# Performance work log

Measured on AMD Instinct MI355X. Metric: run time of the kernel, lower is better.

The kernel has to match this reference:

```python
import jax, jax.numpy as jnp
import numpy as np

D, E, H, K = 1024, 8, 1024, 2          # d_model, num_experts, hidden_size, top_k
NUM_LAYERS, LB_W, Z_W = 16, 0.01, 0.001
B, S = 2, 2048


def setup_inputs() -> dict:
    key = jax.random.key(0)
    ks = jax.random.split(key, 8)
    s = lambda d: 1.0 / np.sqrt(d)
    return {
        "x": jax.random.normal(ks[0], (B, S, D), jnp.float32),
        "w_router": jax.random.normal(ks[1], (D, E), jnp.float32) * s(D),
        "w1": jax.random.normal(ks[2], (E, D, H), jnp.float32) * s(D),
        "w3": jax.random.normal(ks[3], (E, D, H), jnp.float32) * s(D),
        "w2": jax.random.normal(ks[4], (E, H, D), jnp.float32) * s(H),
        "sw1": jax.random.normal(ks[5], (D, H), jnp.float32) * s(D),
        "sw3": jax.random.normal(ks[6], (D, H), jnp.float32) * s(D),
        "sw2": jax.random.normal(ks[7], (H, D), jnp.float32) * s(H),
    }


def reference(x, w_router, w1, w3, w2, sw1, sw3, sw2):
    b, s_len, _ = x.shape
    xt = x.reshape(-1, D)                       # (N, D) flattened tokens
    n_tok = xt.shape[0]

    # ---- router: softmax over experts, then top-k ----
    logits = xt @ w_router                      # (N, E)
    probs = jax.nn.softmax(logits, axis=-1)
    weights, indices = jax.lax.top_k(probs, K)  # (N, K)

    # combine weights scattered back to dense (N, E) form
    onehot = jax.nn.one_hot(indices, E, dtype=x.dtype)    # (N, K, E)
    cw = jnp.einsum("nk,nke->ne", weights, onehot)       # (N, E)
    counts = jnp.sum(onehot, axis=(0, 1))                 # (E,) tokens per expert

    # ---- expert SwiGLU MLPs (dense dispatch, weighted combine) ----
    g = jnp.einsum("nd,edh->neh", xt, w1)                 # (N, E, H)
    u = jnp.einsum("nd,edh->neh", xt, w3)
    h = jax.nn.silu(g) * u
    eout = jnp.einsum("neh,ehd->ned", h, w2)              # (N, E, D)
    out = jnp.einsum("ne,ned->nd", cw, eout)              # (N, D)

    # ---- shared expert, weighted-sum combine with top_k ----
    shared = (jax.nn.silu(xt @ sw1) * (xt @ sw3)) @ sw2   # (N, D)
    out = (out * K + shared) / (K + 1)

    # ---- aux losses (training mode) ----
    logits32 = logits.astype(jnp.float32)
    scale = E * LB_W / (NUM_LAYERS * n_tok * K)
    lb_loss = scale * jnp.dot(counts.astype(jnp.float32),
                              jax.nn.softmax(logits32, axis=-1).sum(axis=0))
    z_loss = jnp.mean(jnp.square(jax.nn.logsumexp(logits32, axis=-1))) * Z_W

    return out.reshape(b, s_len, D), lb_loss, z_loss
```

## Files before the change

### kernel.cpp

```cpp
#include <hip/hip_runtime.h>

#define NTOK 4096
#define NEXP 8
#define MAXTILES 104

typedef __attribute__((ext_vector_type(8))) short short8;
typedef __attribute__((ext_vector_type(4))) float f32x4;
typedef __attribute__((ext_vector_type(4))) unsigned int uint4v;
typedef __attribute__((ext_vector_type(2))) unsigned int uint2v;

__device__ __forceinline__ unsigned short f2bf(float f) {
  union { float f; unsigned u; } v; v.f = f;
  unsigned u = v.u;
  return (unsigned short)((u + 0x7FFFu + ((u >> 16) & 1u)) >> 16);
}

__device__ __forceinline__ void gll16(const void* g, void* l) {
  __builtin_amdgcn_global_load_lds((const __attribute__((address_space(1))) void*)g,
                                   (__attribute__((address_space(3))) void*)l, 16, 0, 0);
}

__global__ __launch_bounds__(256) void cvt_t_all_k(
    const float* __restrict__ w1, const float* __restrict__ w3, const float* __restrict__ w2,
    const float* __restrict__ sw1, const float* __restrict__ sw3, const float* __restrict__ sw2,
    unsigned short* __restrict__ dst ) {
  __shared__ unsigned short tile[64][65];
  int z = blockIdx.z;
  const float* S;
  if (z < 8) S = w1 + (size_t)z * 1048576;
  else if (z < 16) S = w3 + (size_t)(z - 8) * 1048576;
  else if (z < 24) S = w2 + (size_t)(z - 16) * 1048576;
  else S = (z == 24) ? sw1 : (z == 25) ? sw3 : sw2;
  unsigned short* Dp = dst + (size_t)z * 1048576;
  int r0 = blockIdx.y * 64, c0 = blockIdx.x * 64;
  int t = threadIdx.x;
  int r = t >> 2, cb = (t & 3) * 16;
  const float* sp = S + (size_t)(r0 + r) * 1024 + c0 + cb;
  f32x4 v0 = ((const f32x4*)sp)[0], v1 = ((const f32x4*)sp)[1];
  f32x4 v2 = ((const f32x4*)sp)[2], v3 = ((const f32x4*)sp)[3];
#pragma unroll
  for (int j = 0; j < 4; ++j) {
    tile[r][cb + j] = f2bf(v0[j]);
    tile[r][cb + 4 + j] = f2bf(v1[j]);
    tile[r][cb + 8 + j] = f2bf(v2[j]);
    tile[r][cb + 12 + j] = f2bf(v3[j]);
  }
  __syncthreads();
  unsigned short* dp = Dp + (size_t)(c0 + r) * 1024 + r0 + cb;
  uint4v o0, o1;
#pragma unroll
  for (int j = 0; j < 4; ++j) {
    o0[j] = (unsigned)tile[cb + 2 * j][r] | ((unsigned)tile[cb + 2 * j + 1][r] << 16);
    o1[j] = (unsigned)tile[cb + 8 + 2 * j][r] | ((unsigned)tile[cb + 9 + 2 * j][r] << 16);
  }
  ((uint4v*)dp)[0] = o0;
  ((uint4v*)dp)[1] = o1;
}

__global__ __launch_bounds__(256) void router_k(
    const float* __restrict__ x, const float* __restrict__ wr, unsigned short* __restrict__ xb,
    int* __restrict__ rec, float* __restrict__ wts, float* __restrict__ probs,
    float* __restrict__ lsebuf) {
  int t = threadIdx.x, lane = t & 63, wv = t >> 6;
  int tok = blockIdx.x * 4 + wv;
  const f32x4* x4 = (const f32x4*)(x + (size_t)tok * 1024);
  f32x4 xv[4];
#pragma unroll
  for (int j = 0; j < 4; ++j) xv[j] = x4[j * 64 + lane];

  unsigned short* xo = xb + (size_t)tok * 1024;
#pragma unroll
  for (int j = 0; j < 4; ++j) {
    uint2v o;
    o[0] = (unsigned)f2bf(xv[j][0]) | ((unsigned)f2bf(xv[j][1]) << 16);
    o[1] = (unsigned)f2bf(xv[j][2]) | ((unsigned)f2bf(xv[j][3]) << 16);
    *(uint2v*)(xo + j * 256 + lane * 4) = o;
  }

  float acc[NEXP];
#pragma unroll
  for (int e = 0; e < NEXP; ++e) acc[e] = 0.f;
#pragma unroll
  for (int j = 0; j < 4; ++j) {
    int base = j * 256 + lane * 4;
#pragma unroll
    for (int c = 0; c < 4; ++c) {
      float xf = xv[j][c];
      const f32x4* wp = (const f32x4*)(wr + (size_t)(base + c) * NEXP);
      f32x4 w0 = wp[0], w1 = wp[1];
#pragma unroll
      for (int e = 0; e < 4; ++e) { acc[e] += xf * w0[e]; acc[4 + e] += xf * w1[e]; }
    }
  }
#pragma unroll
  for (int off = 32; off > 0; off >>= 1) {
#pragma unroll
    for (int e = 0; e < NEXP; ++e) acc[e] += __shfl_xor(acc[e], off);
  }

  float mx = acc[0];
#pragma unroll
  for (int e = 1; e < NEXP; ++e) mx = fmaxf(mx, acc[e]);
  float s = 0.f;
#pragma unroll
  for (int e = 0; e < NEXP; ++e) s += __expf(acc[e] - mx);
  float inv = 1.f / s;

  if (lane < NEXP) probs[(size_t)tok * NEXP + lane] = __expf(acc[lane] - mx) * inv;
  if (lane == 0) {
    int i0 = 0; float v0 = acc[0];
#pragma unroll
    for (int e = 1; e < NEXP; ++e) if (acc[e] > v0) { v0 = acc[e]; i0 = e; }
    int i1 = -1; float v1 = -3.4e38f;
#pragma unroll
    for (int e = 0; e < NEXP; ++e) if (e != i0 && acc[e] > v1) { v1 = acc[e]; i1 = e; }
    rec[tok] = i0 | (i1 << 8);
    wts[2 * tok] = __expf(v0 - mx) * inv;
    wts[2 * tok + 1] = __expf(v1 - mx) * inv;
    lsebuf[tok] = mx + __logf(s);
  }
}

__global__ __launch_bounds__(256) void build_k(
    const int* __restrict__ rec, const float* __restrict__ wts, const float* __restrict__ probs,
    const float* __restrict__ lsebuf,
    int* __restrict__ tlist, float* __restrict__ wlist,
    int* __restrict__ counts, float* __restrict__ probsum, float* __restrict__ zsum) {
  __shared__ int lcnt[NEXP];
  __shared__ int gbase[NEXP];
  __shared__ float wProb[4][NEXP];
  __shared__ float wZ[4];
  int t = threadIdx.x, lane = t & 63, wv = t >> 6;
  if (t < NEXP) lcnt[t] = 0;
  __syncthreads();

  int tok = blockIdx.x * 256 + t;
  int r = rec[tok];
  int i0 = r & 255, i1 = (r >> 8) & 255;
  float w0 = wts[2 * tok], w1 = wts[2 * tok + 1];
  int p0 = atomicAdd(&lcnt[i0], 1);
  int p1 = atomicAdd(&lcnt[i1], 1);

  f32x4 pr0 = ((const f32x4*)(probs + (size_t)tok * NEXP))[0];
  f32x4 pr1 = ((const f32x4*)(probs + (size_t)tok * NEXP))[1];
  float lv = lsebuf[tok];
  float z = lv * lv;
#pragma unroll
  for (int off = 32; off > 0; off >>= 1) {
#pragma unroll
    for (int c = 0; c < 4; ++c) {
      pr0[c] += __shfl_xor(pr0[c], off);
      pr1[c] += __shfl_xor(pr1[c], off);
    }
    z += __shfl_xor(z, off);
  }
  if (lane == 0) {
#pragma unroll
    for (int c = 0; c < 4; ++c) { wProb[wv][c] = pr0[c]; wProb[wv][4 + c] = pr1[c]; }
    wZ[wv] = z;
  }
  __syncthreads();

  if (t < NEXP) {
    gbase[t] = atomicAdd(&counts[t], lcnt[t]);
    atomicAdd(&probsum[t], wProb[0][t] + wProb[1][t] + wProb[2][t] + wProb[3][t]);
  }
  if (t == 0) atomicAdd(zsum, wZ[0] + wZ[1] + wZ[2] + wZ[3]);
  __syncthreads();

  int q0 = gbase[i0] + p0, q1 = gbase[i1] + p1;
  tlist[i0 * NTOK + q0] = tok;
  wlist[i0 * NTOK + q0] = w0;
  tlist[i1 * NTOK + q1] = tok;
  wlist[i1 * NTOK + q1] = w1;
}

__global__ void scan_k(const int* __restrict__ counts, int* __restrict__ ebase, int* __restrict__ tiles) {
  if (threadIdx.x == 0 && blockIdx.x == 0) {
    int a = 0, t = 0;
    for (int e = 0; e < NEXP; ++e) {
      ebase[e] = a;
      int nt = (counts[e] + 127) >> 7;
      for (int i = 0; i < nt; ++i) tiles[t++] = (e << 16) | i;
      a += nt * 128;
    }
    ebase[NEXP] = a;
    for (int i = 0; i < 32; ++i) tiles[t++] = (NEXP << 16) | i;
    ebase[NEXP + 1] = a + NTOK;
    while (t < MAXTILES) tiles[t++] = -1;
  }
}

__global__ __launch_bounds__(256, 3) void gemm1_k(
    const unsigned short* __restrict__ xb,
    const unsigned short* __restrict__ w1T, const unsigned short* __restrict__ w3T,
    const unsigned short* __restrict__ sw1T, const unsigned short* __restrict__ sw3T,
    unsigned short* __restrict__ hout,
    const int* __restrict__ tlist, const int* __restrict__ counts,
    const int* __restrict__ ebase, const int* __restrict__ tiles) {
  int td = tiles[blockIdx.y];
  if (td < 0) return;
  const int e = td >> 16;
  const int m0 = (td & 0xFFFF) << 7;
  const int n0 = blockIdx.x * 64;
  const bool sh = (e == NEXP);
  const int n_e = sh ? NTOK : counts[e];
  const int hb = ebase[e];
  const unsigned short* B1p = sh ? sw1T : w1T + (size_t)e * 1048576;
  const unsigned short* B3p = sh ? sw3T : w3T + (size_t)e * 1048576;
  const int* listp = tlist + e * NTOK;

  __shared__ unsigned short As[128 * 64], Bs1[64 * 64], Bs3[64 * 64];
  const int tid = threadIdx.x, lane = tid & 63, wv = tid >> 6;
  const int wrw = wv >> 1, wc = wv & 1, l16 = lane & 15, lq = lane >> 4;

  const unsigned short* ga[4];
#pragma unroll
  for (int i = 0; i < 4; ++i) {
    int c = tid + i * 256;
    int r = c >> 3, ks = (c & 7) ^ (r & 7);
    int ar = m0 + r;
    int rowA = sh ? ar : (ar < n_e ? (listp[ar] & 0xFFFF) : 0);
    ga[i] = xb + (size_t)rowA * 1024 + ks * 8;
  }
  const unsigned short* gb[2];
  const unsigned short* gc[2];
#pragma unroll
  for (int i = 0; i < 2; ++i) {
    int c = tid + i * 256;
    int r = c >> 3, ks = (c & 7) ^ (r & 7);
    gb[i] = B1p + (size_t)(n0 + r) * 1024 + ks * 8;
    gc[i] = B3p + (size_t)(n0 + r) * 1024 + ks * 8;
  }
  unsigned short* lA[4];
#pragma unroll
  for (int i = 0; i < 4; ++i) lA[i] = As + i * 2048 + wv * 512;
  unsigned short* lB[2] = {Bs1 + wv * 512, Bs1 + 2048 + wv * 512};
  unsigned short* lC[2] = {Bs3 + wv * 512, Bs3 + 2048 + wv * 512};

  f32x4 accg[4][2], accu[4][2];
#pragma unroll
  for (int mi = 0; mi < 4; ++mi)
#pragma unroll
    for (int ni = 0; ni < 2; ++ni)
#pragma unroll
      for (int r = 0; r < 4; ++r) { accg[mi][ni][r] = 0.f; accu[mi][ni][r] = 0.f; }

  for (int k0 = 0; k0 < 1024; k0 += 64) {
#pragma unroll
    for (int i = 0; i < 4; ++i) { gll16(ga[i], lA[i]); ga[i] += 64; }
#pragma unroll
    for (int i = 0; i < 2; ++i) { gll16(gb[i], lB[i]); gb[i] += 64; gll16(gc[i], lC[i]); gc[i] += 64; }
    __syncthreads();
#pragma unroll
    for (int kh = 0; kh < 2; ++kh) {
      short8 af[4], b1f[2], b3f[2];
#pragma unroll
      for (int mi = 0; mi < 4; ++mi) {
        int R = wrw * 64 + mi * 16 + l16;
        int s = (kh * 4 + lq) ^ (R & 7);
        af[mi] = *(const short8*)&As[R * 64 + s * 8];
      }
#pragma unroll
      for (int ni = 0; ni < 2; ++ni) {
        int R = wc * 32 + ni * 16 + l16;
        int s = (kh * 4 + lq) ^ (R & 7);
        b1f[ni] = *(const short8*)&Bs1[R * 64 + s * 8];
        b3f[ni] = *(const short8*)&Bs3[R * 64 + s * 8];
      }
#pragma unroll
      for (int mi = 0; mi < 4; ++mi)
#pragma unroll
        for (int ni = 0; ni < 2; ++ni) {
          accg[mi][ni] = __builtin_amdgcn_mfma_f32_16x16x32_bf16(af[mi], b1f[ni], accg[mi][ni], 0, 0, 0);
          accu[mi][ni] = __builtin_amdgcn_mfma_f32_16x16x32_bf16(af[mi], b3f[ni], accu[mi][ni], 0, 0, 0);
        }
    }
    __syncthreads();
  }

#pragma unroll
  for (int mi = 0; mi < 4; ++mi)
#pragma unroll
    for (int ni = 0; ni < 2; ++ni) {
      int col = n0 + wc * 32 + ni * 16 + l16;
#pragma unroll
      for (int r = 0; r < 4; ++r) {
        int row = m0 + wrw * 64 + mi * 16 + lq * 4 + r;
        float g = accg[mi][ni][r], u = accu[mi][ni][r];
        float h = g / (1.f + __expf(-g)) * u;
        hout[(size_t)(hb + row) * 1024 + col] = (row < n_e) ? f2bf(h) : (unsigned short)0;
      }
    }
}

__global__ __launch_bounds__(256, 3) void gemm2_k(
    const unsigned short* __restrict__ hbuf,
    const unsigned short* __restrict__ w2T, const unsigned short* __restrict__ sw2T,
    float* __restrict__ out,
    const int* __restrict__ tlist, const float* __restrict__ wlist,
    const int* __restrict__ counts, const int* __restrict__ ebase, const int* __restrict__ tiles) {
  int td = tiles[blockIdx.y];
  if (td < 0) return;
  const int e = td >> 16;
  const int m0 = (td & 0xFFFF) << 7;
  const int n0 = blockIdx.x * 128;
  const bool sh = (e == NEXP);
  const int n_e = sh ? NTOK : counts[e];
  const int hb = ebase[e];
  const unsigned short* Bp = sh ? sw2T : w2T + (size_t)e * 1048576;
  const int* listp = tlist + e * NTOK;

  __shared__ unsigned short As[128 * 64], Bs[128 * 64];
  const int tid = threadIdx.x, lane = tid & 63, wv = tid >> 6;
  const int wrw = wv >> 1, wc = wv & 1, l16 = lane & 15, lq = lane >> 4;

  const unsigned short* ga[4];
  const unsigned short* gb[4];
#pragma unroll
  for (int i = 0; i < 4; ++i) {
    int c = tid + i * 256;
    int r = c >> 3, ks = (c & 7) ^ (r & 7);
    ga[i] = hbuf + (size_t)(hb + m0 + r) * 1024 + ks * 8;
    gb[i] = Bp + (size_t)(n0 + r) * 1024 + ks * 8;
  }
  unsigned short* lA[4];
  unsigned short* lB[4];
#pragma unroll
  for (int i = 0; i < 4; ++i) {
    lA[i] = As + i * 2048 + wv * 512;
    lB[i] = Bs + i * 2048 + wv * 512;
  }

  f32x4 acc[4][4];
#pragma unroll
  for (int mi = 0; mi < 4; ++mi)
#pragma unroll
    for (int ni = 0; ni < 4; ++ni)
#pragma unroll
      for (int r = 0; r < 4; ++r) acc[mi][ni][r] = 0.f;

  for (int k0 = 0; k0 < 1024; k0 += 64) {
#pragma unroll
    for (int i = 0; i < 4; ++i) {
      gll16(ga[i], lA[i]); ga[i] += 64;
      gll16(gb[i], lB[i]); gb[i] += 64;
    }
    __syncthreads();
#pragma unroll
    for (int kh = 0; kh < 2; ++kh) {
      short8 af[4], bf[4];
#pragma unroll
      for (int mi = 0; mi < 4; ++mi) {
        int R = wrw * 64 + mi * 16 + l16;
        int s = (kh * 4 + lq) ^ (R & 7);
        af[mi] = *(const short8*)&As[R * 64 + s * 8];
      }
#pragma unroll
      for (int ni = 0; ni < 4; ++ni) {
        int R = wc * 64 + ni * 16 + l16;
        int s = (kh * 4 + lq) ^ (R & 7);
        bf[ni] = *(const short8*)&Bs[R * 64 + s * 8];
      }
#pragma unroll
      for (int mi = 0; mi < 4; ++mi)
#pragma unroll
        for (int ni = 0; ni < 4; ++ni)
          acc[mi][ni] = __builtin_amdgcn_mfma_f32_16x16x32_bf16(af[mi], bf[ni], acc[mi][ni], 0, 0, 0);
    }
    __syncthreads();
  }

#pragma unroll
  for (int mi = 0; mi < 4; ++mi)
#pragma unroll
    for (int r = 0; r < 4; ++r) {
      int row = m0 + wrw * 64 + mi * 16 + lq * 4 + r;
      if (sh) {
        float* yp = out + (size_t)row * 1024 + n0 + wc * 64 + l16;
#pragma unroll
        for (int ni = 0; ni < 4; ++ni) atomicAdd(&yp[ni * 16], acc[mi][ni][r] * (1.f / 3.f));
      } else if (row < n_e) {
        int tok = listp[row] & 0xFFFF;
        float wt = wlist[e * NTOK + row] * (2.f / 3.f);
        float* yp = out + (size_t)tok * 1024 + n0 + wc * 64 + l16;
#pragma unroll
        for (int ni = 0; ni < 4; ++ni) atomicAdd(&yp[ni * 16], wt * acc[mi][ni][r]);
      }
    }
}

__global__ void losses_k(const int* __restrict__ counts, const float* __restrict__ probsum,
                         const float* __restrict__ zsum, float* __restrict__ out) {
  if (threadIdx.x == 0 && blockIdx.x == 0) {
    float dot = 0.f;
    for (int e = 0; e < NEXP; ++e) dot += (float)counts[e] * probsum[e];
    out[0] = 6.103515625e-7f * dot;
    out[1] = zsum[0] * (0.001f / 4096.f);
  }
}

extern "C" void kernel_launch(void* const* d_in, const int* in_sizes, int n_in,
                              void* d_out, int out_size, void* d_ws, size_t ws_size,
                              hipStream_t stream) {
  const float* x   = (const float*)d_in[0];
  const float* wrt = (const float*)d_in[1];
  const float* w1  = (const float*)d_in[2];
  const float* w3  = (const float*)d_in[3];
  const float* w2  = (const float*)d_in[4];
  const float* sw1 = (const float*)d_in[5];
  const float* sw3 = (const float*)d_in[6];
  const float* sw2 = (const float*)d_in[7];
  float* out = (float*)d_out;

  char* p = (char*)d_ws;
  auto alloc = [&](size_t b) { char* r = p; p += (b + 255) & ~(size_t)255; return r; };
  unsigned short* xb   = (unsigned short*)alloc((size_t)NTOK * 1024 * 2);
  unsigned short* w1T  = (unsigned short*)alloc((size_t)27 * 1048576 * 2);
  unsigned short* w3T  = w1T + (size_t)8 * 1048576;
  unsigned short* w2T  = w3T + (size_t)8 * 1048576;
  unsigned short* sw1T = w2T + (size_t)8 * 1048576;
  unsigned short* sw3T = sw1T + 1048576;
  unsigned short* sw2T = sw3T + 1048576;
  unsigned short* hbuf = (unsigned short*)alloc((size_t)13312 * 1024 * 2);
  int* tlist    = (int*)alloc((size_t)NEXP * NTOK * 4);
  float* wlist  = (float*)alloc((size_t)NEXP * NTOK * 4);
  int* rec      = (int*)alloc((size_t)NTOK * 4);
  float* wts    = (float*)alloc((size_t)NTOK * 2 * 4);
  float* probs  = (float*)alloc((size_t)NTOK * NEXP * 4);
  float* lsebuf = (float*)alloc((size_t)NTOK * 4);
  int* tiles    = (int*)alloc(MAXTILES * 4);
  int* ebase    = (int*)alloc(256);
  char* stats   = alloc(768);
  int* counts   = (int*)stats;
  float* probsum = (float*)(stats + 256);
  float* zsum    = (float*)(stats + 512);

  (void)hipMemsetAsync(stats, 0, 768, stream);
  (void)hipMemsetAsync(out, 0, (size_t)out_size * 4, stream);

  cvt_t_all_k<<<dim3(16, 16, 27), 256, 0, stream>>>(w1, w3, w2, sw1, sw3, sw2, w1T);
  router_k<<<1024, 256, 0, stream>>>(x, wrt, xb, rec, wts, probs, lsebuf);
  build_k<<<16, 256, 0, stream>>>(rec, wts, probs, lsebuf, tlist, wlist, counts, probsum, zsum);
  scan_k<<<1, 64, 0, stream>>>(counts, ebase, tiles);
  gemm1_k<<<dim3(16, MAXTILES), 256, 0, stream>>>(xb, w1T, w3T, sw1T, sw3T, hbuf, tlist, counts, ebase, tiles);
  gemm2_k<<<dim3(8, MAXTILES), 256, 0, stream>>>(hbuf, w2T, sw2T, out, tlist, wlist, counts, ebase, tiles);
  losses_k<<<1, 64, 0, stream>>>(counts, probsum, zsum, out + (size_t)NTOK * 1024);
}
```

Measured before the change: 326.7 us.

## Fuse prep kernels, single-block routing build, replace atomic combine with staged sum

Merges weight conversion and the router into one launch, and folds the build, scan and loss kernels into a single 1024-thread block. This drops the memsets and several small launches. gemm2 no longer does float atomicAdds into the output. It writes each of the top-k and shared contributions to a separate slice of a 3-slot fp32 buffer, and a new combine kernel sums them. The aim is to remove atomic contention and launch overhead, at the cost of writing and reading an extra 48MB buffer. The single-block build also serialises the routing scatter.

```diff
diff --git a/kernel.cpp b/kernel.cpp
--- a/kernel.cpp
+++ b/kernel.cpp
@@ -20,174 +20,174 @@
                                    (__attribute__((address_space(3))) void*)l, 16, 0, 0);
 }
 
-__global__ __launch_bounds__(256) void cvt_t_all_k(
+__global__ __launch_bounds__(256) void prep_k(
     const float* __restrict__ w1, const float* __restrict__ w3, const float* __restrict__ w2,
     const float* __restrict__ sw1, const float* __restrict__ sw3, const float* __restrict__ sw2,
-    unsigned short* __restrict__ dst ) {
-  __shared__ unsigned short tile[64][65];
-  int z = blockIdx.z;
-  const float* S;
-  if (z < 8) S = w1 + (size_t)z * 1048576;
-  else if (z < 16) S = w3 + (size_t)(z - 8) * 1048576;
-  else if (z < 24) S = w2 + (size_t)(z - 16) * 1048576;
-  else S = (z == 24) ? sw1 : (z == 25) ? sw3 : sw2;
-  unsigned short* Dp = dst + (size_t)z * 1048576;
-  int r0 = blockIdx.y * 64, c0 = blockIdx.x * 64;
-  int t = threadIdx.x;
-  int r = t >> 2, cb = (t & 3) * 16;
-  const float* sp = S + (size_t)(r0 + r) * 1024 + c0 + cb;
-  f32x4 v0 = ((const f32x4*)sp)[0], v1 = ((const f32x4*)sp)[1];
-  f32x4 v2 = ((const f32x4*)sp)[2], v3 = ((const f32x4*)sp)[3];
-#pragma unroll
-  for (int j = 0; j < 4; ++j) {
-    tile[r][cb + j] = f2bf(v0[j]);
-    tile[r][cb + 4 + j] = f2bf(v1[j]);
-    tile[r][cb + 8 + j] = f2bf(v2[j]);
-    tile[r][cb + 12 + j] = f2bf(v3[j]);
-  }
-  __syncthreads();
-  unsigned short* dp = Dp + (size_t)(c0 + r) * 1024 + r0 + cb;
-  uint4v o0, o1;
-#pragma unroll
-  for (int j = 0; j < 4; ++j) {
-    o0[j] = (unsigned)tile[cb + 2 * j][r] | ((unsigned)tile[cb + 2 * j + 1][r] << 16);
-    o1[j] = (unsigned)tile[cb + 8 + 2 * j][r] | ((unsigned)tile[cb + 9 + 2 * j][r] << 16);
-  }
-  ((uint4v*)dp)[0] = o0;
-  ((uint4v*)dp)[1] = o1;
-}
-
-__global__ __launch_bounds__(256) void router_k(
+    unsigned short* __restrict__ dst,
     const float* __restrict__ x, const float* __restrict__ wr, unsigned short* __restrict__ xb,
     int* __restrict__ rec, float* __restrict__ wts, float* __restrict__ probs,
     float* __restrict__ lsebuf) {
-  int t = threadIdx.x, lane = t & 63, wv = t >> 6;
-  int tok = blockIdx.x * 4 + wv;
-  const f32x4* x4 = (const f32x4*)(x + (size_t)tok * 1024);
-  f32x4 xv[4];
-#pragma unroll
-  for (int j = 0; j < 4; ++j) xv[j] = x4[j * 64 + lane];
-
-  unsigned short* xo = xb + (size_t)tok * 1024;
-#pragma unroll
-  for (int j = 0; j < 4; ++j) {
-    uint2v o;
-    o[0] = (unsigned)f2bf(xv[j][0]) | ((unsigned)f2bf(xv[j][1]) << 16);
-    o[1] = (unsigned)f2bf(xv[j][2]) | ((unsigned)f2bf(xv[j][3]) << 16);
-    *(uint2v*)(xo + j * 256 + lane * 4) = o;
-  }
-
-  float acc[NEXP];
-#pragma unroll
-  for (int e = 0; e < NEXP; ++e) acc[e] = 0.f;
-#pragma unroll
-  for (int j = 0; j < 4; ++j) {
-    int base = j * 256 + lane * 4;
-#pragma unroll
-    for (int c = 0; c < 4; ++c) {
-      float xf = xv[j][c];
-      const f32x4* wp = (const f32x4*)(wr + (size_t)(base + c) * NEXP);
-      f32x4 w0 = wp[0], w1 = wp[1];
-#pragma unroll
-      for (int e = 0; e < 4; ++e) { acc[e] += xf * w0[e]; acc[4 + e] += xf * w1[e]; }
-    }
-  }
-#pragma unroll
-  for (int off = 32; off > 0; off >>= 1) {
-#pragma unroll
-    for (int e = 0; e < NEXP; ++e) acc[e] += __shfl_xor(acc[e], off);
-  }
-
-  float mx = acc[0];
-#pragma unroll
-  for (int e = 1; e < NEXP; ++e) mx = fmaxf(mx, acc[e]);
-  float s = 0.f;
-#pragma unroll
-  for (int e = 0; e < NEXP; ++e) s += __expf(acc[e] - mx);
-  float inv = 1.f / s;
-
-  if (lane < NEXP) probs[(size_t)tok * NEXP + lane] = __expf(acc[lane] - mx) * inv;
-  if (lane == 0) {
-    int i0 = 0; float v0 = acc[0];
-#pragma unroll
-    for (int e = 1; e < NEXP; ++e) if (acc[e] > v0) { v0 = acc[e]; i0 = e; }
-    int i1 = -1; float v1 = -3.4e38f;
-#pragma unroll
-    for (int e = 0; e < NEXP; ++e) if (e != i0 && acc[e] > v1) { v1 = acc[e]; i1 = e; }
-    rec[tok] = i0 | (i1 << 8);
-    wts[2 * tok] = __expf(v0 - mx) * inv;
-    wts[2 * tok + 1] = __expf(v1 - mx) * inv;
-    lsebuf[tok] = mx + __logf(s);
-  }
-}
-
-__global__ __launch_bounds__(256) void build_k(
+  __shared__ unsigned short tile[64][65];
+  int b = blockIdx.x;
+  if (b < 6912) {
+    int z = b >> 8, rem = b & 255;
+    int r0 = (rem >> 4) * 64, c0 = (rem & 15) * 64;
+    const float* S;
+    if (z < 8) S = w1 + (size_t)z * 1048576;
+    else if (z < 16) S = w3 + (size_t)(z - 8) * 1048576;
+    else if (z < 24) S = w2 + (size_t)(z - 16) * 1048576;
+    else S = (z == 24) ? sw1 : (z == 25) ? sw3 : sw2;
+    unsigned short* Dp = dst + (size_t)z * 1048576;
+    int t = threadIdx.x;
+    int r = t >> 2, cb = (t & 3) * 16;
+    const float* sp = S + (size_t)(r0 + r) * 1024 + c0 + cb;
+    f32x4 v0 = ((const f32x4*)sp)[0], v1 = ((const f32x4*)sp)[1];
+    f32x4 v2 = ((const f32x4*)sp)[2], v3 = ((const f32x4*)sp)[3];
+#pragma unroll
+    for (int j = 0; j < 4; ++j) {
+      tile[r][cb + j] = f2bf(v0[j]);
+      tile[r][cb + 4 + j] = f2bf(v1[j]);
+      tile[r][cb + 8 + j] = f2bf(v2[j]);
+      tile[r][cb + 12 + j] = f2bf(v3[j]);
+    }
+    __syncthreads();
+    unsigned short* dp = Dp + (size_t)(c0 + r) * 1024 + r0 + cb;
+    uint4v o0, o1;
+#pragma unroll
+    for (int j = 0; j < 4; ++j) {
+      o0[j] = (unsigned)tile[cb + 2 * j][r] | ((unsigned)tile[cb + 2 * j + 1][r] << 16);
+      o1[j] = (unsigned)tile[cb + 8 + 2 * j][r] | ((unsigned)tile[cb + 9 + 2 * j][r] << 16);
+    }
+    ((uint4v*)dp)[0] = o0;
+    ((uint4v*)dp)[1] = o1;
+  } else {
+    int t = threadIdx.x, lane = t & 63, wv = t >> 6;
+    int tok = (b - 6912) * 4 + wv;
+    const f32x4* x4 = (const f32x4*)(x + (size_t)tok * 1024);
+    f32x4 xv[4];
+#pragma unroll
+    for (int j = 0; j < 4; ++j) xv[j] = x4[j * 64 + lane];
+
+    unsigned short* xo = xb + (size_t)tok * 1024;
+#pragma unroll
+    for (int j = 0; j < 4; ++j) {
+      uint2v o;
+      o[0] = (unsigned)f2bf(xv[j][0]) | ((unsigned)f2bf(xv[j][1]) << 16);
+      o[1] = (unsigned)f2bf(xv[j][2]) | ((unsigned)f2bf(xv[j][3]) << 16);
+      *(uint2v*)(xo + j * 256 + lane * 4) = o;
+    }
+
+    float acc[NEXP];
+#pragma unroll
+    for (int e = 0; e < NEXP; ++e) acc[e] = 0.f;
+#pragma unroll
+    for (int j = 0; j < 4; ++j) {
+      int base = j * 256 + lane * 4;
+#pragma unroll
+      for (int c = 0; c < 4; ++c) {
+        float xf = xv[j][c];
+        const f32x4* wp = (const f32x4*)(wr + (size_t)(base + c) * NEXP);
+        f32x4 q0 = wp[0], q1 = wp[1];
+#pragma unroll
+        for (int e = 0; e < 4; ++e) { acc[e] += xf * q0[e]; acc[4 + e] += xf * q1[e]; }
+      }
+    }
+#pragma unroll
+    for (int off = 32; off > 0; off >>= 1) {
+#pragma unroll
+      for (int e = 0; e < NEXP; ++e) acc[e] += __shfl_xor(acc[e], off);
+    }
+
+    float mx = acc[0];
+#pragma unroll
+    for (int e = 1; e < NEXP; ++e) mx = fmaxf(mx, acc[e]);
+    float s = 0.f;
+#pragma unroll
+    for (int e = 0; e < NEXP; ++e) s += __expf(acc[e] - mx);
+    float inv = 1.f / s;
+
+    if (lane < NEXP) probs[(size_t)tok * NEXP + lane] = __expf(acc[lane] - mx) * inv;
+    if (lane == 0) {
+      int i0 = 0; float v0 = acc[0];
+#pragma unroll
+      for (int e = 1; e < NEXP; ++e) if (acc[e] > v0) { v0 = acc[e]; i0 = e; }
+      int i1 = -1; float v1 = -3.4e38f;
+#pragma unroll
+      for (int e = 0; e < NEXP; ++e) if (e != i0 && acc[e] > v1) { v1 = acc[e]; i1 = e; }
+      rec[tok] = i0 | (i1 << 8);
+      wts[2 * tok] = __expf(v0 - mx) * inv;
+      wts[2 * tok + 1] = __expf(v1 - mx) * inv;
+      lsebuf[tok] = mx + __logf(s);
+    }
+  }
+}
+
+__global__ __launch_bounds__(1024) void build_k(
     const int* __restrict__ rec, const float* __restrict__ wts, const float* __restrict__ probs,
     const float* __restrict__ lsebuf,
     int* __restrict__ tlist, float* __restrict__ wlist,
-    int* __restrict__ counts, float* __restrict__ probsum, float* __restrict__ zsum) {
+    int* __restrict__ counts, int* __restrict__ ebase, int* __restrict__ tiles,
+    float* __restrict__ lossout) {
   __shared__ int lcnt[NEXP];
-  __shared__ int gbase[NEXP];
-  __shared__ float wProb[4][NEXP];
-  __shared__ float wZ[4];
-  int t = threadIdx.x, lane = t & 63, wv = t >> 6;
-  if (t < NEXP) lcnt[t] = 0;
+  __shared__ float sprob[NEXP];
+  __shared__ float sz;
+  int t = threadIdx.x, lane = t & 63;
+  if (t < NEXP) { lcnt[t] = 0; sprob[t] = 0.f; }
+  if (t == 0) sz = 0.f;
   __syncthreads();
 
-  int tok = blockIdx.x * 256 + t;
-  int r = rec[tok];
-  int i0 = r & 255, i1 = (r >> 8) & 255;
-  float w0 = wts[2 * tok], w1 = wts[2 * tok + 1];
-  int p0 = atomicAdd(&lcnt[i0], 1);
-  int p1 = atomicAdd(&lcnt[i1], 1);
-
-  f32x4 pr0 = ((const f32x4*)(probs + (size_t)tok * NEXP))[0];
-  f32x4 pr1 = ((const f32x4*)(probs + (size_t)tok * NEXP))[1];
-  float lv = lsebuf[tok];
-  float z = lv * lv;
+  float pacc[NEXP];
+#pragma unroll
+  for (int e = 0; e < NEXP; ++e) pacc[e] = 0.f;
+  float zacc = 0.f;
+
+#pragma unroll
+  for (int it = 0; it < 4; ++it) {
+    int tok = t + it * 1024;
+    int r = rec[tok];
+    int i0 = r & 255, i1 = (r >> 8) & 255;
+    int p0 = atomicAdd(&lcnt[i0], 1);
+    tlist[i0 * NTOK + p0] = tok;
+    wlist[i0 * NTOK + p0] = wts[2 * tok];
+    int p1 = atomicAdd(&lcnt[i1], 1);
+    tlist[i1 * NTOK + p1] = tok | (1 << 16);
+    wlist[i1 * NTOK + p1] = wts[2 * tok + 1];
+    f32x4 a = ((const f32x4*)(probs + (size_t)tok * NEXP))[0];
+    f32x4 c = ((const f32x4*)(probs + (size_t)tok * NEXP))[1];
+#pragma unroll
+    for (int j = 0; j < 4; ++j) { pacc[j] += a[j]; pacc[4 + j] += c[j]; }
+    float lv = lsebuf[tok];
+    zacc += lv * lv;
+  }
 #pragma unroll
   for (int off = 32; off > 0; off >>= 1) {
 #pragma unroll
-    for (int c = 0; c < 4; ++c) {
-      pr0[c] += __shfl_xor(pr0[c], off);
-      pr1[c] += __shfl_xor(pr1[c], off);
-    }
-    z += __shfl_xor(z, off);
+    for (int e = 0; e < NEXP; ++e) pacc[e] += __shfl_xor(pacc[e], off);
+    zacc += __shfl_xor(zacc, off);
   }
   if (lane == 0) {
 #pragma unroll
-    for (int c = 0; c < 4; ++c) { wProb[wv][c] = pr0[c]; wProb[wv][4 + c] = pr1[c]; }
-    wZ[wv] = z;
+    for (int e = 0; e < NEXP; ++e) atomicAdd(&sprob[e], pacc[e]);
+    atomicAdd(&sz, zacc);
   }
   __syncthreads();
 
-  if (t < NEXP) {
-    gbase[t] = atomicAdd(&counts[t], lcnt[t]);
-    atomicAdd(&probsum[t], wProb[0][t] + wProb[1][t] + wProb[2][t] + wProb[3][t]);
-  }
-  if (t == 0) atomicAdd(zsum, wZ[0] + wZ[1] + wZ[2] + wZ[3]);
-  __syncthreads();
-
-  int q0 = gbase[i0] + p0, q1 = gbase[i1] + p1;
-  tlist[i0 * NTOK + q0] = tok;
-  wlist[i0 * NTOK + q0] = w0;
-  tlist[i1 * NTOK + q1] = tok;
-  wlist[i1 * NTOK + q1] = w1;
-}
-
-__global__ void scan_k(const int* __restrict__ counts, int* __restrict__ ebase, int* __restrict__ tiles) {
-  if (threadIdx.x == 0 && blockIdx.x == 0) {
-    int a = 0, t = 0;
+  if (t == 0) {
+    int a = 0, tt = 0;
+    float dot = 0.f;
     for (int e = 0; e < NEXP; ++e) {
+      counts[e] = lcnt[e];
       ebase[e] = a;
-      int nt = (counts[e] + 127) >> 7;
-      for (int i = 0; i < nt; ++i) tiles[t++] = (e << 16) | i;
+      int nt = (lcnt[e] + 127) >> 7;
+      for (int i = 0; i < nt; ++i) tiles[tt++] = (e << 16) | i;
       a += nt * 128;
+      dot += (float)lcnt[e] * sprob[e];
     }
     ebase[NEXP] = a;
-    for (int i = 0; i < 32; ++i) tiles[t++] = (NEXP << 16) | i;
-    ebase[NEXP + 1] = a + NTOK;
-    while (t < MAXTILES) tiles[t++] = -1;
+    for (int i = 0; i < 32; ++i) tiles[tt++] = (NEXP << 16) | i;
+    while (tt < MAXTILES) tiles[tt++] = -1;
+    lossout[0] = 6.103515625e-7f * dot;
+    lossout[1] = sz * (0.001f / 4096.f);
   }
 }
 
@@ -297,7 +297,7 @@
 __global__ __launch_bounds__(256, 3) void gemm2_k(
     const unsigned short* __restrict__ hbuf,
     const unsigned short* __restrict__ w2T, const unsigned short* __restrict__ sw2T,
-    float* __restrict__ out,
+    float* __restrict__ yout,
     const int* __restrict__ tlist, const float* __restrict__ wlist,
     const int* __restrict__ counts, const int* __restrict__ ebase, const int* __restrict__ tiles) {
   int td = tiles[blockIdx.y];
@@ -377,27 +377,27 @@
     for (int r = 0; r < 4; ++r) {
       int row = m0 + wrw * 64 + mi * 16 + lq * 4 + r;
       if (sh) {
-        float* yp = out + (size_t)row * 1024 + n0 + wc * 64 + l16;
-#pragma unroll
-        for (int ni = 0; ni < 4; ++ni) atomicAdd(&yp[ni * 16], acc[mi][ni][r] * (1.f / 3.f));
+        float* yp = yout + ((size_t)2 * NTOK + row) * 1024 + n0 + wc * 64 + l16;
+#pragma unroll
+        for (int ni = 0; ni < 4; ++ni) yp[ni * 16] = acc[mi][ni][r] * (1.f / 3.f);
       } else if (row < n_e) {
-        int tok = listp[row] & 0xFFFF;
+        int ent = listp[row];
         float wt = wlist[e * NTOK + row] * (2.f / 3.f);
-        float* yp = out + (size_t)tok * 1024 + n0 + wc * 64 + l16;
-#pragma unroll
-        for (int ni = 0; ni < 4; ++ni) atomicAdd(&yp[ni * 16], wt * acc[mi][ni][r]);
-      }
-    }
-}
-
-__global__ void losses_k(const int* __restrict__ counts, const float* __restrict__ probsum,
-                         const float* __restrict__ zsum, float* __restrict__ out) {
-  if (threadIdx.x == 0 && blockIdx.x == 0) {
-    float dot = 0.f;
-    for (int e = 0; e < NEXP; ++e) dot += (float)counts[e] * probsum[e];
-    out[0] = 6.103515625e-7f * dot;
-    out[1] = zsum[0] * (0.001f / 4096.f);
-  }
+        int tok = ent & 0xFFFF, ks = ent >> 16;
+        float* yp = yout + ((size_t)ks * NTOK + tok) * 1024 + n0 + wc * 64 + l16;
+#pragma unroll
+        for (int ni = 0; ni < 4; ++ni) yp[ni * 16] = wt * acc[mi][ni][r];
+      }
+    }
+}
+
+__global__ __launch_bounds__(256) void combine_k(const float* __restrict__ y,
+                                                 float* __restrict__ out) {
+  size_t i = (size_t)blockIdx.x * 256 + threadIdx.x;
+  const f32x4* y0 = (const f32x4*)y + i;
+  const f32x4* y1 = y0 + (NTOK * 1024 / 4);
+  const f32x4* y2 = y1 + (NTOK * 1024 / 4);
+  ((f32x4*)out)[i] = *y0 + *y1 + *y2;
 }
 
 extern "C" void kernel_launch(void* const* d_in, const int* in_sizes, int n_in,
@@ -423,6 +423,7 @@
   unsigned short* sw3T = sw1T + 1048576;
   unsigned short* sw2T = sw3T + 1048576;
   unsigned short* hbuf = (unsigned short*)alloc((size_t)13312 * 1024 * 2);
+  float* ybuf   = (float*)alloc((size_t)3 * NTOK * 1024 * 4);
   int* tlist    = (int*)alloc((size_t)NEXP * NTOK * 4);
   float* wlist  = (float*)alloc((size_t)NEXP * NTOK * 4);
   int* rec      = (int*)alloc((size_t)NTOK * 4);
@@ -431,19 +432,13 @@
   float* lsebuf = (float*)alloc((size_t)NTOK * 4);
   int* tiles    = (int*)alloc(MAXTILES * 4);
   int* ebase    = (int*)alloc(256);
-  char* stats   = alloc(768);
-  int* counts   = (int*)stats;
-  float* probsum = (float*)(stats + 256);
-  float* zsum    = (float*)(stats + 512);
-
-  (void)hipMemsetAsync(stats, 0, 768, stream);
-  (void)hipMemsetAsync(out, 0, (size_t)out_size * 4, stream);
-
-  cvt_t_all_k<<<dim3(16, 16, 27), 256, 0, stream>>>(w1, w3, w2, sw1, sw3, sw2, w1T);
-  router_k<<<1024, 256, 0, stream>>>(x, wrt, xb, rec, wts, probs, lsebuf);
-  build_k<<<16, 256, 0, stream>>>(rec, wts, probs, lsebuf, tlist, wlist, counts, probsum, zsum);
-  scan_k<<<1, 64, 0, stream>>>(counts, ebase, tiles);
+  int* counts   = (int*)alloc(256);
+
+  prep_k<<<7936, 256, 0, stream>>>(w1, w3, w2, sw1, sw3, sw2, w1T,
+                                   x, wrt, xb, rec, wts, probs, lsebuf);
+  build_k<<<1, 1024, 0, stream>>>(rec, wts, probs, lsebuf, tlist, wlist,
+                                  counts, ebase, tiles, out + (size_t)NTOK * 1024);
   gemm1_k<<<dim3(16, MAXTILES), 256, 0, stream>>>(xb, w1T, w3T, sw1T, sw3T, hbuf, tlist, counts, ebase, tiles);
-  gemm2_k<<<dim3(8, MAXTILES), 256, 0, stream>>>(hbuf, w2T, sw2T, out, tlist, wlist, counts, ebase, tiles);
-  losses_k<<<1, 64, 0, stream>>>(counts, probsum, zsum, out + (size_t)NTOK * 1024);
-}
+  gemm2_k<<<dim3(8, MAXTILES), 256, 0, stream>>>(hbuf, w2T, sw2T, ybuf, tlist, wlist, counts, ebase, tiles);
+  combine_k<<<NTOK * 1024 / 4 / 256, 256, 0, stream>>>(ybuf, out);
+}
```

New measurement: 315.8 us. 1.03x faster.
